# Kernel optimization log

Hardware: AMD Instinct MI355X
Metric: run time of the kernel (lower is better)

Reference implementation:

```python
import math
import jax, jax.numpy as jnp
import numpy as np

LOW_FREQ = 1
FACTOR = 1


def setup_inputs() -> dict:
    key = jax.random.key(0)
    x = jax.random.normal(key, (8, 4096, 512), dtype=jnp.float32)
    return {"x": x}


def reference(x):
    b, t, d = x.shape
    x_freq = jnp.fft.rfft(x, axis=1)  # (b, t//2+1, d) complex
    if t % 2 == 0:
        x_freq = x_freq[:, LOW_FREQ:-1]
        f = jnp.fft.rfftfreq(t)[LOW_FREQ:-1]
    else:
        x_freq = x_freq[:, LOW_FREQ:]
        f = jnp.fft.rfftfreq(t)[LOW_FREQ:]
    length = x_freq.shape[1]
    top_k = int(FACTOR * math.log(length))

    # top-k |X(f)| independently per (batch, channel)
    amp_all = jnp.abs(x_freq)                      # (b, F, d)
    _, idx = jax.lax.top_k(jnp.transpose(amp_all, (0, 2, 1)), top_k)  # (b, d, k)
    idx = jnp.transpose(idx, (0, 2, 1))            # (b, k, d)
    x_sel = jnp.take_along_axis(x_freq, idx, axis=1)  # (b, k, d) complex
    f_sel = f[idx].astype(jnp.float32)             # (b, k, d)

    # extrapolate: append conjugate components with negated frequency
    x2 = jnp.concatenate([x_sel, jnp.conj(x_sel)], axis=1)  # (b, 2k, d)
    f2 = jnp.concatenate([f_sel, -f_sel], axis=1)           # (b, 2k, d)
    amp = jnp.abs(x2)[:, :, None, :]               # (b, 2k, 1, d)
    phase = jnp.angle(x2)[:, :, None, :]           # (b, 2k, 1, d)
    tt = jnp.arange(t, dtype=jnp.float32)[None, None, :, None]  # (1,1,t,1)
    x_time = amp * jnp.cos(2.0 * math.pi * f2[:, :, None, :] * tt + phase)  # (b,2k,t,d)
    return jnp.sum(x_time, axis=1)                 # (b, t, d)
```

## Files before the change

### kernel.cpp

```cpp
#include <hip/hip_runtime.h>
#include <math.h>

#define B 8
#define T 4096
#define D 512
#define NPAIR ((B * D) / 2)
#define TOPK 7
#define PAD(e) ((e) + ((e) >> 4))

__device__ __forceinline__ int drev(int k) {
  return ((k & 15) << 8) | (k & 240) | (k >> 8);
}

__device__ __forceinline__ float2 cmul(float2 a, float2 b) {
  return make_float2(a.x * b.x - a.y * b.y, a.x * b.y + a.y * b.x);
}
__device__ __forceinline__ float2 cadd(float2 a, float2 b) { return make_float2(a.x + b.x, a.y + b.y); }
__device__ __forceinline__ float2 csub(float2 a, float2 b) { return make_float2(a.x - b.x, a.y - b.y); }
__device__ __forceinline__ float2 cmul_negi(float2 a) { return make_float2(a.y, -a.x); }

__device__ __forceinline__ void dft4(float2& a, float2& b, float2& c, float2& d) {
  const float2 t0 = cadd(a, c), t1 = csub(a, c);
  const float2 t2 = cadd(b, d), t3n = cmul_negi(csub(b, d));
  a = cadd(t0, t2);
  b = cadd(t1, t3n);
  c = csub(t0, t2);
  d = csub(t1, t3n);
}

#define C16 0.92387953251f
#define S16 0.38268343236f
#define RS2 0.70710678119f
__device__ __forceinline__ void dft16(float2 r[16]) {
  dft4(r[0], r[4], r[8],  r[12]);
  dft4(r[1], r[5], r[9],  r[13]);
  dft4(r[2], r[6], r[10], r[14]);
  dft4(r[3], r[7], r[11], r[15]);
  const float2 W1 = make_float2(C16, -S16);
  const float2 W2 = make_float2(RS2, -RS2);
  const float2 W3 = make_float2(S16, -C16);
  const float2 W6 = make_float2(-RS2, -RS2);
  const float2 W9 = make_float2(-C16, S16);
  r[5]  = cmul(r[5],  W1);
  r[9]  = cmul(r[9],  W2);
  r[13] = cmul(r[13], W3);
  r[6]  = cmul(r[6],  W2);
  r[10] = cmul_negi(r[10]);
  r[14] = cmul(r[14], W6);
  r[7]  = cmul(r[7],  W3);
  r[11] = cmul(r[11], W6);
  r[15] = cmul(r[15], W9);
  dft4(r[0],  r[1],  r[2],  r[3]);
  dft4(r[4],  r[5],  r[6],  r[7]);
  dft4(r[8],  r[9],  r[10], r[11]);
  dft4(r[12], r[13], r[14], r[15]);
}
#define SW4(k) ((((k) & 3) << 2) | ((k) >> 2))

__global__ __launch_bounds__(256) void k_transpose_pack(const float* __restrict__ x,
                                                        float2* __restrict__ xp) {
  __shared__ float tT[64][65];
  const int b  = blockIdx.z;
  const int t0 = blockIdx.x * 64;
  const int d0 = blockIdx.y * 64;
  const int tid = threadIdx.x;

  const int c4 = tid & 15;
  const int r0 = tid >> 4;
  for (int r = r0; r < 64; r += 16) {
    const float4 v = *(const float4*)&x[((size_t)b * T + (t0 + r)) * D + d0 + 4 * c4];
    tT[4 * c4 + 0][r] = v.x;
    tT[4 * c4 + 1][r] = v.y;
    tT[4 * c4 + 2][r] = v.z;
    tT[4 * c4 + 3][r] = v.w;
  }
  __syncthreads();

  const int tt  = tid & 31;
  const int rp0 = tid >> 5;
  for (int rp = rp0; rp < 32; rp += 8) {
    const float2 a  = *(const float2*)&tT[2 * rp][2 * tt];
    const float2 bb = *(const float2*)&tT[2 * rp + 1][2 * tt];
    const float4 o = make_float4(a.x, bb.x, a.y, bb.y);
    *(float4*)&xp[((size_t)b * (D / 2) + (d0 / 2 + rp)) * T + t0 + 2 * tt] = o;
  }
}

__global__ __launch_bounds__(256) void k_fft_topk(float2* __restrict__ xp) {
  __shared__ float2 Z[PAD(T - 1) + 1];
  __shared__ float  s_rv[2][4];
  __shared__ int    s_rk[2][4];
  __shared__ float4 s_cf[2 * TOPK];

  const int tid = threadIdx.x;
  float2* g = xp + (size_t)blockIdx.x * T;

  float2 r[16];
  #pragma unroll
  for (int a = 0; a < 16; ++a) r[a] = g[(a << 8) + tid];

  dft16(r);
  {
    float s, c;
    __sincosf(6.283185307179586f / 4096.0f * (float)tid, &s, &c);
    const float2 w = make_float2(c, -s);
    float2 t = make_float2(1.0f, 0.0f);
    Z[PAD(tid)] = r[0];
    #pragma unroll
    for (int k1 = 1; k1 < 16; ++k1) {
      t = cmul(t, w);
      Z[PAD((k1 << 8) + tid)] = cmul(r[SW4(k1)], t);
    }
  }
  __syncthreads();

  {
    const int m1 = tid & 15;
    const int base = ((tid >> 4) << 8) + m1;
    #pragma unroll
    for (int m2 = 0; m2 < 16; ++m2) r[m2] = Z[PAD(base + (m2 << 4))];
    dft16(r);
    float s, c;
    __sincosf(6.283185307179586f / 256.0f * (float)m1, &s, &c);
    const float2 w = make_float2(c, -s);
    float2 t = make_float2(1.0f, 0.0f);
    Z[PAD(base)] = r[0];
    #pragma unroll
    for (int p = 1; p < 16; ++p) {
      t = cmul(t, w);
      Z[PAD(base + (p << 4))] = cmul(r[SW4(p)], t);
    }
  }
  __syncthreads();

  {
    const int base = tid << 4;
    #pragma unroll
    for (int m1 = 0; m1 < 16; ++m1) r[m1] = Z[PAD(base + m1)];
    dft16(r);
    #pragma unroll
    for (int q = 0; q < 16; ++q) Z[PAD(base + q)] = r[SW4(q)];
  }
  __syncthreads();

  float a1v[8], a2v[8];
  #pragma unroll
  for (int j = 0; j < 8; ++j) {
    const int k = 1 + tid + (j << 8);
    if (k >= T / 2) { a1v[j] = -1e30f; a2v[j] = -1e30f; continue; }
    const float2 zk = Z[PAD(drev(k))];
    const float2 zn = Z[PAD(drev(T - k))];
    const float x1r = 0.5f * (zk.x + zn.x), x1i = 0.5f * (zk.y - zn.y);
    const float x2r = 0.5f * (zk.y + zn.y), x2i = 0.5f * (zn.x - zk.x);
    a1v[j] = x1r * x1r + x1i * x1i;
    a2v[j] = x2r * x2r + x2i * x2i;
  }

  for (int sh = 0; sh < 2; ++sh) {
    for (int it = 0; it < TOPK; ++it) {
      const int buf = (sh * TOPK + it) & 1;
      float bv = -1e30f;
      int bj = 0;
      #pragma unroll
      for (int j = 0; j < 8; ++j) {
        const float v = (sh == 0) ? a1v[j] : a2v[j];
        if (v > bv) { bv = v; bj = j; }
      }
      int bk = 1 + tid + (bj << 8);
      #pragma unroll
      for (int off = 1; off < 64; off <<= 1) {
        const float ov = __shfl_xor(bv, off);
        const int   ok = __shfl_xor(bk, off);
        if (ov > bv || (ov == bv && ok < bk)) { bv = ov; bk = ok; }
      }
      if ((tid & 63) == 0) { s_rv[buf][tid >> 6] = bv; s_rk[buf][tid >> 6] = bk; }
      __syncthreads();
      float wv = s_rv[buf][0];
      int   wk = s_rk[buf][0];
      #pragma unroll
      for (int w = 1; w < 4; ++w) {
        const float ov = s_rv[buf][w];
        const int   ok = s_rk[buf][w];
        if (ov > wv || (ov == wv && ok < wk)) { wv = ov; wk = ok; }
      }
      if (((wk - 1) & 255) == tid) {
        const int j = (wk - 1) >> 8;
        #pragma unroll
        for (int jj = 0; jj < 8; ++jj)
          if (jj == j) { if (sh == 0) a1v[jj] = -1e30f; else a2v[jj] = -1e30f; }
      }
      if (tid == 0) {
        const float2 zk = Z[PAD(drev(wk))];
        const float2 zn = Z[PAD(drev(T - wk))];
        float re, im;
        if (sh == 0) { re = 0.5f * (zk.x + zn.x); im = 0.5f * (zk.y - zn.y); }
        else         { re = 0.5f * (zk.y + zn.y); im = 0.5f * (zn.x - zk.x); }
        s_cf[sh * TOPK + it] = make_float4((float)wk, re, im, 0.0f);
      }
    }
  }
  __syncthreads();

  float4* cf = (float4*)g;
  if (tid < 2 * TOPK) cf[tid] = s_cf[tid];
}

__global__ __launch_bounds__(256) void k_eval(const float* __restrict__ ws,
                                              float* __restrict__ out) {
  __shared__ float  tile[64][64];
  __shared__ float4 s_coef[64 * TOPK];

  const int tid = threadIdx.x;
  const int b   = blockIdx.z;
  const int d0  = blockIdx.y * 64;
  const int t0  = blockIdx.x * 64;

  for (int idx = tid; idx < 64 * TOPK; idx += 256) {
    const int s = idx / TOPK, j = idx - s * TOPK;
    const int P = (b * D + d0) / 2 + (s >> 1);
    const int sh = s & 1;
    s_coef[idx] = ((const float4*)(ws + (size_t)P * (2 * T)))[sh * TOPK + j];
  }
  __syncthreads();

  const int dl = tid & 63;
  const int tg = tid >> 6;
  const float w0 = 6.283185307179586f / 4096.0f;

  float re[TOPK], im[TOPK], cc[TOPK], ss[TOPK], cd[TOPK], sd[TOPK];
  const int ts = t0 + tg;
  #pragma unroll
  for (int j = 0; j < TOPK; ++j) {
    const float4 v = s_coef[dl * TOPK + j];
    const int k = (int)v.x;
    re[j] = 2.0f * v.y;
    im[j] = 2.0f * v.z;
    const float a0 = w0 * (float)((k * ts) & (T - 1));
    const float ad = w0 * (float)((4 * k) & (T - 1));
    ss[j] = __sinf(a0); cc[j] = __cosf(a0);
    sd[j] = __sinf(ad); cd[j] = __cosf(ad);
  }

  #pragma unroll
  for (int i = 0; i < 16; ++i) {
    float acc = 0.0f;
    #pragma unroll
    for (int j = 0; j < TOPK; ++j) {
      acc += re[j] * cc[j] - im[j] * ss[j];
      const float nc = cc[j] * cd[j] - ss[j] * sd[j];
      const float ns = ss[j] * cd[j] + cc[j] * sd[j];
      cc[j] = nc; ss[j] = ns;
    }
    tile[tg + 4 * i][dl] = acc;
  }
  __syncthreads();

  const int c4 = tid & 15;
  const int rw = tid >> 4;
  for (int rr = rw; rr < 64; rr += 16) {
    const float4 v = *(const float4*)&tile[rr][4 * c4];
    *(float4*)&out[((size_t)b * T + (t0 + rr)) * D + d0 + 4 * c4] = v;
  }
}

extern "C" void kernel_launch(void* const* d_in, const int* in_sizes, int n_in,
                              void* d_out, int out_size, void* d_ws, size_t ws_size,
                              hipStream_t stream) {
  const float* x = (const float*)d_in[0];
  float* out = (float*)d_out;
  float2* xp = (float2*)d_ws;

  dim3 tgrid(T / 64, D / 64, B);
  hipLaunchKernelGGL(k_transpose_pack, tgrid, dim3(256), 0, stream, x, xp);
  hipLaunchKernelGGL(k_fft_topk, dim3(NPAIR), dim3(256), 0, stream, xp);
  hipLaunchKernelGGL(k_eval, tgrid, dim3(256), 0, stream, (const float*)d_ws, out);
}
```

Baseline: 198.1 us.

## Make top-k selection wave-local with one block barrier, extend LDS padding

Each wave now finds its own top-7 candidates for both signal halves with interleaved shuffle reductions, and needs no block barriers for this. Two waves then merge the 28 per-wave candidates per half, replacing fourteen block-wide barriers with one. The merge is exact because the global top-7 must lie within the union of each wave's top-7. The shared-memory padding also gains an extra term for every 256 elements, to reduce bank conflicts in the strided FFT passes, at the cost of slightly more LDS.

```diff
diff --git a/kernel.cpp b/kernel.cpp
--- a/kernel.cpp
+++ b/kernel.cpp
@@ -6,7 +6,7 @@
 #define D 512
 #define NPAIR ((B * D) / 2)
 #define TOPK 7
-#define PAD(e) ((e) + ((e) >> 4))
+#define PAD(e) ((e) + ((e) >> 4) + ((e) >> 8))
 
 __device__ __forceinline__ int drev(int k) {
   return ((k & 15) << 8) | (k & 240) | (k >> 8);
@@ -88,11 +88,12 @@
 
 __global__ __launch_bounds__(256) void k_fft_topk(float2* __restrict__ xp) {
   __shared__ float2 Z[PAD(T - 1) + 1];
-  __shared__ float  s_rv[2][4];
-  __shared__ int    s_rk[2][4];
-  __shared__ float4 s_cf[2 * TOPK];
-
-  const int tid = threadIdx.x;
+  __shared__ float  s_cv[2][4][8];
+  __shared__ int    s_ck[2][4][8];
+
+  const int tid  = threadIdx.x;
+  const int lane = tid & 63;
+  const int wid  = tid >> 6;
   float2* g = xp + (size_t)blockIdx.x * T;
 
   float2 r[16];
@@ -156,53 +157,70 @@
     a2v[j] = x2r * x2r + x2i * x2i;
   }
 
-  for (int sh = 0; sh < 2; ++sh) {
+  #pragma unroll
+  for (int it = 0; it < TOPK; ++it) {
+    float bv0 = -1e30f, bv1 = -1e30f;
+    int bj0 = 0, bj1 = 0;
+    #pragma unroll
+    for (int j = 0; j < 8; ++j) {
+      if (a1v[j] > bv0) { bv0 = a1v[j]; bj0 = j; }
+      if (a2v[j] > bv1) { bv1 = a2v[j]; bj1 = j; }
+    }
+    int bk0 = 1 + tid + (bj0 << 8);
+    int bk1 = 1 + tid + (bj1 << 8);
+    #pragma unroll
+    for (int off = 1; off < 64; off <<= 1) {
+      const float ov0 = __shfl_xor(bv0, off);
+      const int   ok0 = __shfl_xor(bk0, off);
+      const float ov1 = __shfl_xor(bv1, off);
+      const int   ok1 = __shfl_xor(bk1, off);
+      if (ov0 > bv0 || (ov0 == bv0 && ok0 < bk0)) { bv0 = ov0; bk0 = ok0; }
+      if (ov1 > bv1 || (ov1 == bv1 && ok1 < bk1)) { bv1 = ov1; bk1 = ok1; }
+    }
+    if (lane == 0) {
+      s_cv[0][wid][it] = bv0; s_ck[0][wid][it] = bk0;
+      s_cv[1][wid][it] = bv1; s_ck[1][wid][it] = bk1;
+    }
+    if (((bk0 - 1) & 255) == tid) {
+      const int j = (bk0 - 1) >> 8;
+      #pragma unroll
+      for (int jj = 0; jj < 8; ++jj) if (jj == j) a1v[jj] = -1e30f;
+    }
+    if (((bk1 - 1) & 255) == tid) {
+      const int j = (bk1 - 1) >> 8;
+      #pragma unroll
+      for (int jj = 0; jj < 8; ++jj) if (jj == j) a2v[jj] = -1e30f;
+    }
+  }
+  __syncthreads();
+
+  if (wid < 2) {
+    const int sh = wid;
+    const int w  = (lane >> 3) & 3;
+    const int i  = lane & 7;
+    float cv = (i < TOPK) ? s_cv[sh][w][i] : -1e30f;
+    int   ck = (i < TOPK) ? s_ck[sh][w][i] : 0x7fffffff;
+    float4* cf = (float4*)g;
+    #pragma unroll
     for (int it = 0; it < TOPK; ++it) {
-      const int buf = (sh * TOPK + it) & 1;
-      float bv = -1e30f;
-      int bj = 0;
-      #pragma unroll
-      for (int j = 0; j < 8; ++j) {
-        const float v = (sh == 0) ? a1v[j] : a2v[j];
-        if (v > bv) { bv = v; bj = j; }
-      }
-      int bk = 1 + tid + (bj << 8);
+      float bv = cv; int bk = ck;
       #pragma unroll
       for (int off = 1; off < 64; off <<= 1) {
         const float ov = __shfl_xor(bv, off);
         const int   ok = __shfl_xor(bk, off);
         if (ov > bv || (ov == bv && ok < bk)) { bv = ov; bk = ok; }
       }
-      if ((tid & 63) == 0) { s_rv[buf][tid >> 6] = bv; s_rk[buf][tid >> 6] = bk; }
-      __syncthreads();
-      float wv = s_rv[buf][0];
-      int   wk = s_rk[buf][0];
-      #pragma unroll
-      for (int w = 1; w < 4; ++w) {
-        const float ov = s_rv[buf][w];
-        const int   ok = s_rk[buf][w];
-        if (ov > wv || (ov == wv && ok < wk)) { wv = ov; wk = ok; }
-      }
-      if (((wk - 1) & 255) == tid) {
-        const int j = (wk - 1) >> 8;
-        #pragma unroll
-        for (int jj = 0; jj < 8; ++jj)
-          if (jj == j) { if (sh == 0) a1v[jj] = -1e30f; else a2v[jj] = -1e30f; }
-      }
-      if (tid == 0) {
-        const float2 zk = Z[PAD(drev(wk))];
-        const float2 zn = Z[PAD(drev(T - wk))];
+      if (lane == it) {
+        const float2 zk = Z[PAD(drev(bk))];
+        const float2 zn = Z[PAD(drev(T - bk))];
         float re, im;
         if (sh == 0) { re = 0.5f * (zk.x + zn.x); im = 0.5f * (zk.y - zn.y); }
         else         { re = 0.5f * (zk.y + zn.y); im = 0.5f * (zn.x - zk.x); }
-        s_cf[sh * TOPK + it] = make_float4((float)wk, re, im, 0.0f);
+        cf[sh * TOPK + it] = make_float4((float)bk, re, im, 0.0f);
       }
-    }
-  }
-  __syncthreads();
-
-  float4* cf = (float4*)g;
-  if (tid < 2 * TOPK) cf[tid] = s_cf[tid];
+      if (ck == bk) cv = -1e30f;
+    }
+  }
 }
 
 __global__ __launch_bounds__(256) void k_eval(const float* __restrict__ ws,
```

Result: no change. 196.9 us (-0.6%).

## Split top-k selection across waves with packed 64-bit keys and bitonic merge

Applied to the files above, without the earlier changes.

Top-k selection no longer runs as 14 block-wide iterations, each with a __syncthreads. Instead, two waves handle each of the two packed signals. Each wave finds its local top-7 using 64-bit keys that pack magnitude and inverted index, then a single wave bitonic-sorts the 14 candidates to get the final 7. This removes most of the block barriers and shared-memory reductions in the selection phase. The LDS padding also gains an extra >>8 term to reduce bank conflicts in the FFT stages, at the cost of slightly more shared memory.

```diff
diff --git a/kernel.cpp b/kernel.cpp
--- a/kernel.cpp
+++ b/kernel.cpp
@@ -6,7 +6,7 @@
 #define D 512
 #define NPAIR ((B * D) / 2)
 #define TOPK 7
-#define PAD(e) ((e) + ((e) >> 4))
+#define PAD(e) ((e) + ((e) >> 4) + ((e) >> 8))
 
 __device__ __forceinline__ int drev(int k) {
   return ((k & 15) << 8) | (k & 240) | (k >> 8);
@@ -18,6 +18,12 @@
 __device__ __forceinline__ float2 cadd(float2 a, float2 b) { return make_float2(a.x + b.x, a.y + b.y); }
 __device__ __forceinline__ float2 csub(float2 a, float2 b) { return make_float2(a.x - b.x, a.y - b.y); }
 __device__ __forceinline__ float2 cmul_negi(float2 a) { return make_float2(a.y, -a.x); }
+
+__device__ __forceinline__ unsigned long long shfl_xor_u64(unsigned long long v, int off) {
+  const unsigned lo = __shfl_xor((unsigned)v, off);
+  const unsigned hi = __shfl_xor((unsigned)(v >> 32), off);
+  return ((unsigned long long)hi << 32) | lo;
+}
 
 __device__ __forceinline__ void dft4(float2& a, float2& b, float2& c, float2& d) {
   const float2 t0 = cadd(a, c), t1 = csub(a, c);
@@ -88,11 +94,11 @@
 
 __global__ __launch_bounds__(256) void k_fft_topk(float2* __restrict__ xp) {
   __shared__ float2 Z[PAD(T - 1) + 1];
-  __shared__ float  s_rv[2][4];
-  __shared__ int    s_rk[2][4];
-  __shared__ float4 s_cf[2 * TOPK];
-
-  const int tid = threadIdx.x;
+  __shared__ unsigned long long s_cand[2][2][8];
+
+  const int tid  = threadIdx.x;
+  const int lane = tid & 63;
+  const int wid  = tid >> 6;
   float2* g = xp + (size_t)blockIdx.x * T;
 
   float2 r[16];
@@ -143,66 +149,68 @@
   }
   __syncthreads();
 
-  float a1v[8], a2v[8];
-  #pragma unroll
-  for (int j = 0; j < 8; ++j) {
-    const int k = 1 + tid + (j << 8);
-    if (k >= T / 2) { a1v[j] = -1e30f; a2v[j] = -1e30f; continue; }
+  const int sh = wid >> 1;
+  const int u  = ((wid & 1) << 6) | lane;
+  unsigned long long key[16];
+  #pragma unroll
+  for (int j = 0; j < 16; ++j) {
+    const int k = 1 + u + (j << 7);
+    if (k >= T / 2) { key[j] = 0ull; continue; }
     const float2 zk = Z[PAD(drev(k))];
     const float2 zn = Z[PAD(drev(T - k))];
-    const float x1r = 0.5f * (zk.x + zn.x), x1i = 0.5f * (zk.y - zn.y);
-    const float x2r = 0.5f * (zk.y + zn.y), x2i = 0.5f * (zn.x - zk.x);
-    a1v[j] = x1r * x1r + x1i * x1i;
-    a2v[j] = x2r * x2r + x2i * x2i;
-  }
-
-  for (int sh = 0; sh < 2; ++sh) {
-    for (int it = 0; it < TOPK; ++it) {
-      const int buf = (sh * TOPK + it) & 1;
-      float bv = -1e30f;
-      int bj = 0;
+    float re, im;
+    if (sh == 0) { re = zk.x + zn.x; im = zk.y - zn.y; }
+    else         { re = zk.y + zn.y; im = zn.x - zk.x; }
+    const float a = re * re + im * im;
+    key[j] = ((unsigned long long)(__float_as_uint(a) | 0x80000000u) << 32)
+           | (unsigned)(0xFFFFu ^ k);
+  }
+
+  #pragma unroll
+  for (int it = 0; it < TOPK; ++it) {
+    unsigned long long m = key[0];
+    #pragma unroll
+    for (int j = 1; j < 16; ++j) m = (key[j] > m) ? key[j] : m;
+    #pragma unroll
+    for (int off = 1; off < 64; off <<= 1) {
+      const unsigned long long o = shfl_xor_u64(m, off);
+      m = (o > m) ? o : m;
+    }
+    #pragma unroll
+    for (int j = 0; j < 16; ++j)
+      if (key[j] == m) key[j] = 0ull;
+    if (lane == 0) s_cand[sh][wid & 1][it] = m;
+  }
+  __syncthreads();
+
+  if ((wid & 1) == 0) {
+    const int sh2 = wid >> 1;
+    const int w   = (lane >> 3) & 1;
+    const int i   = lane & 7;
+    unsigned long long kk =
+        (lane < 16 && i < TOPK) ? s_cand[sh2][w][i] : 0ull;
+    #pragma unroll
+    for (int ksz = 2; ksz <= 16; ksz <<= 1) {
       #pragma unroll
-      for (int j = 0; j < 8; ++j) {
-        const float v = (sh == 0) ? a1v[j] : a2v[j];
-        if (v > bv) { bv = v; bj = j; }
+      for (int j = ksz >> 1; j > 0; j >>= 1) {
+        const unsigned long long o = shfl_xor_u64(kk, j);
+        const bool dirDesc = ((lane & ksz) == 0);
+        const bool lower   = ((lane & j) == 0);
+        const unsigned long long big = (kk > o) ? kk : o;
+        const unsigned long long sml = (kk > o) ? o : kk;
+        kk = (lower == dirDesc) ? big : sml;
       }
-      int bk = 1 + tid + (bj << 8);
-      #pragma unroll
-      for (int off = 1; off < 64; off <<= 1) {
-        const float ov = __shfl_xor(bv, off);
-        const int   ok = __shfl_xor(bk, off);
-        if (ov > bv || (ov == bv && ok < bk)) { bv = ov; bk = ok; }
-      }
-      if ((tid & 63) == 0) { s_rv[buf][tid >> 6] = bv; s_rk[buf][tid >> 6] = bk; }
-      __syncthreads();
-      float wv = s_rv[buf][0];
-      int   wk = s_rk[buf][0];
-      #pragma unroll
-      for (int w = 1; w < 4; ++w) {
-        const float ov = s_rv[buf][w];
-        const int   ok = s_rk[buf][w];
-        if (ov > wv || (ov == wv && ok < wk)) { wv = ov; wk = ok; }
-      }
-      if (((wk - 1) & 255) == tid) {
-        const int j = (wk - 1) >> 8;
-        #pragma unroll
-        for (int jj = 0; jj < 8; ++jj)
-          if (jj == j) { if (sh == 0) a1v[jj] = -1e30f; else a2v[jj] = -1e30f; }
-      }
-      if (tid == 0) {
-        const float2 zk = Z[PAD(drev(wk))];
-        const float2 zn = Z[PAD(drev(T - wk))];
-        float re, im;
-        if (sh == 0) { re = 0.5f * (zk.x + zn.x); im = 0.5f * (zk.y - zn.y); }
-        else         { re = 0.5f * (zk.y + zn.y); im = 0.5f * (zn.x - zk.x); }
-        s_cf[sh * TOPK + it] = make_float4((float)wk, re, im, 0.0f);
-      }
-    }
-  }
-  __syncthreads();
-
-  float4* cf = (float4*)g;
-  if (tid < 2 * TOPK) cf[tid] = s_cf[tid];
+    }
+    if (lane < TOPK) {
+      const int k = 0xFFFF ^ (int)(kk & 0xFFFFull);
+      const float2 zk = Z[PAD(drev(k))];
+      const float2 zn = Z[PAD(drev(T - k))];
+      float re, im;
+      if (sh2 == 0) { re = 0.5f * (zk.x + zn.x); im = 0.5f * (zk.y - zn.y); }
+      else          { re = 0.5f * (zk.y + zn.y); im = 0.5f * (zn.x - zk.x); }
+      ((float4*)g)[sh2 * TOPK + lane] = make_float4((float)k, re, im, 0.0f);
+    }
+  }
 }
 
 __global__ __launch_bounds__(256) void k_eval(const float* __restrict__ ws,
```

After: 175.7 us. 11.3% less time.
